# Optimization experiments

Hardware: AMD Instinct MI355X
Metric: run time of the kernel (lower is better)

The kernel has to match this reference:

```python
import jax, jax.numpy as jnp
import numpy as np

P_DROP = 0.2
N_NODES = 100000
N_EDGES = 1600000
IN_DIM, HID_DIM, OUT_DIM = 128, 128, 64


def sage_conv(x, src, dst, Wl, Wr, b, n_nodes):
    # PyG SAGEConv (aggr='mean', root_weight=True):
    #   out_i = W_l @ mean_{j in N(i)} x_j + W_r @ x_i + b
    msgs = jnp.take(x, src, axis=0)                                   # [E, d]
    agg = jax.ops.segment_sum(msgs, dst, num_segments=n_nodes)        # [N, d]
    cnt = jax.ops.segment_sum(jnp.ones((src.shape[0],), x.dtype), dst,
                              num_segments=n_nodes)                   # [N]
    agg = agg / jnp.maximum(cnt, 1.0)[:, None]                        # mean, 0 for isolated nodes
    return agg @ Wl + x @ Wr + b


def setup_inputs() -> dict:
    key = jax.random.key(0)
    ks = jax.random.split(key, 8)
    x = jax.random.normal(ks[0], (N_NODES, IN_DIM), dtype=jnp.float32)
    edge_index = jax.random.randint(ks[1], (2, N_EDGES), 0, N_NODES, dtype=jnp.int32)
    drop_u = jax.random.uniform(ks[2], (N_NODES, HID_DIM), dtype=jnp.float32)
    s1 = 1.0 / np.sqrt(IN_DIM)
    s2 = 1.0 / np.sqrt(HID_DIM)
    W1l = jax.random.normal(ks[3], (IN_DIM, HID_DIM), dtype=jnp.float32) * s1
    W1r = jax.random.normal(ks[4], (IN_DIM, HID_DIM), dtype=jnp.float32) * s1
    b1 = jnp.zeros((HID_DIM,), dtype=jnp.float32)
    W2l = jax.random.normal(ks[5], (HID_DIM, OUT_DIM), dtype=jnp.float32) * s2
    W2r = jax.random.normal(ks[6], (HID_DIM, OUT_DIM), dtype=jnp.float32) * s2
    b2 = jnp.zeros((OUT_DIM,), dtype=jnp.float32)
    return {"x": x, "edge_index": edge_index, "drop_u": drop_u,
            "W1l": W1l, "W1r": W1r, "b1": b1,
            "W2l": W2l, "W2r": W2r, "b2": b2}


def reference(x, edge_index, drop_u, W1l, W1r, b1, W2l, W2r, b2):
    n = x.shape[0]
    src, dst = edge_index[0], edge_index[1]
    h = jax.nn.elu(sage_conv(x, src, dst, W1l, W1r, b1, n))
    keep = (drop_u >= P_DROP).astype(h.dtype) / (1.0 - P_DROP)  # inverted dropout, p=0.2
    h = h * keep
    h = jax.nn.elu(sage_conv(h, src, dst, W2l, W2r, b2, n))
    return h
```

## Files before the change

kernel.cpp:

```cpp
#include <hip/hip_runtime.h>
#include <cstdint>
#include <cstddef>

#define TPB 256
#define BCAP 2560
#define NBKMAX 800
#define EPB 8192

typedef short bf16x8 __attribute__((ext_vector_type(8)));
typedef float f32x4 __attribute__((ext_vector_type(4)));

__device__ __forceinline__ unsigned short f2bf(float f) {
  unsigned int u = __float_as_uint(f);
  unsigned int r = (u + 0x7fffu + ((u >> 16) & 1u)) >> 16;
  return (unsigned short)r;
}
__device__ __forceinline__ float bf2f(unsigned short h) {
  return __uint_as_float(((unsigned int)h) << 16);
}

__device__ __forceinline__ void gload16(const void* g, void* l) {
  __builtin_amdgcn_global_load_lds(
      (const __attribute__((address_space(1))) unsigned int*)g,
      (__attribute__((address_space(3))) unsigned int*)l, 16, 0, 0);
}

template <int N>
__device__ __forceinline__ void waitvm() {
  asm volatile("s_waitcnt vmcnt(%0)" ::"n"(N) : "memory");
}


__global__ __launch_bounds__(256) void multisplit_scatter(
    const int* __restrict__ src, const int* __restrict__ dst,
    unsigned int* __restrict__ be, int* __restrict__ bcnt, int e, int nbk) {
  __shared__ int hist[NBKMAX];
  __shared__ int curs[NBKMAX];
  int tx = threadIdx.x;
  int e0 = blockIdx.x * EPB;
  int e1 = min(e, e0 + EPB);

  for (int b = tx; b < nbk; b += TPB) hist[b] = 0;
  __syncthreads();
  for (int i = e0 + tx; i < e1; i += TPB) atomicAdd(&hist[dst[i] >> 7], 1);
  __syncthreads();
  int rot = (blockIdx.x * 131) % nbk;
  for (int s = tx; s < nbk; s += TPB) {
    int b = s + rot;
    if (b >= nbk) b -= nbk;
    int h = hist[b];
    curs[b] = (h > 0) ? atomicAdd(&bcnt[b], h) : 0;
  }
  __syncthreads();
  for (int i = e0 + tx; i < e1; i += TPB) {
    int d = dst[i];
    int b = d >> 7;
    int p = atomicAdd(&curs[b], 1);
    if (p < BCAP)
      be[(size_t)b * BCAP + p] = ((unsigned int)(d & 127) << 17) | (unsigned int)src[i];
  }
}

__global__ void bucket_scan(const int* __restrict__ bcnt, int* __restrict__ bbase, int nbk) {
  __shared__ int s[TPB];
  __shared__ int carry;
  int tx = threadIdx.x;
  if (tx == 0) carry = 0;
  __syncthreads();
  for (int base = 0; base < nbk; base += TPB) {
    int i = base + tx;
    int v = (i < nbk) ? bcnt[i] : 0;
    s[tx] = v;
    __syncthreads();
    for (int d = 1; d < TPB; d <<= 1) {
      int t = (tx >= d) ? s[tx - d] : 0;
      __syncthreads();
      s[tx] += t;
      __syncthreads();
    }
    int c = carry;
    if (i < nbk) bbase[i] = c + s[tx] - v;
    __syncthreads();
    if (tx == TPB - 1) carry = c + s[tx];
    __syncthreads();
  }
}

__global__ __launch_bounds__(256) void per_bucket_build(
    const unsigned int* __restrict__ be, const int* __restrict__ bcnt,
    const int* __restrict__ bbase, int* __restrict__ off, int* __restrict__ col,
    int n, int e) {
  int b = blockIdx.x, tx = threadIdx.x;
  int cnt = bcnt[b];
  if (cnt > BCAP) cnt = BCAP;
  int base = bbase[b];
  int node0 = b << 7;
  __shared__ int scnt[128];
  __shared__ int sscan[128];
  if (tx < 128) scnt[tx] = 0;
  __syncthreads();
  const unsigned int* eb = be + (size_t)b * BCAP;
  for (int i = tx; i < cnt; i += 256) atomicAdd(&scnt[eb[i] >> 17], 1);
  __syncthreads();
  if (tx < 128) sscan[tx] = scnt[tx];
  __syncthreads();
  for (int d = 1; d < 128; d <<= 1) {
    int t = 0;
    if (tx < 128 && tx >= d) t = sscan[tx - d];
    __syncthreads();
    if (tx < 128) sscan[tx] += t;
    __syncthreads();
  }
  if (tx < 128) {
    int excl = sscan[tx] - scnt[tx];
    if (node0 + tx < n) off[node0 + tx] = base + excl;
    scnt[tx] = excl;
  }
  if (b == 0 && tx == 0) off[n] = e;
  __syncthreads();
  for (int i = tx; i < cnt; i += 256) {
    unsigned int u = eb[i];
    int p = atomicAdd(&scnt[u >> 17], 1);
    col[base + p] = (int)(u & 0x1ffff);
  }
}


__global__ void f32_to_bf16_v4(const float* __restrict__ in, unsigned short* __restrict__ out,
                               int n4) {
  int i = blockIdx.x * TPB + threadIdx.x;
  if (i >= n4) return;
  float4 v = ((const float4*)in)[i];
  ushort4 o;
  o.x = f2bf(v.x); o.y = f2bf(v.y); o.z = f2bf(v.z); o.w = f2bf(v.w);
  ((ushort4*)out)[i] = o;
}

__global__ void make_dropmask(const float* __restrict__ u, unsigned char* __restrict__ m,
                              int n4) {
  int i = blockIdx.x * TPB + threadIdx.x;
  if (i >= n4) return;
  float4 v = ((const float4*)u)[i];
  uchar4 o;
  o.x = (v.x >= 0.2f) ? 1 : 0;
  o.y = (v.y >= 0.2f) ? 1 : 0;
  o.z = (v.z >= 0.2f) ? 1 : 0;
  o.w = (v.w >= 0.2f) ? 1 : 0;
  ((uchar4*)m)[i] = o;
}

template <int NF>
__global__ void build_wt(const float* __restrict__ Wl, const float* __restrict__ Wr,
                         unsigned short* __restrict__ Wt) {
  int idx = blockIdx.x * TPB + threadIdx.x;
  if (idx >= NF * 256) return;
  int nn = idx >> 8;
  int k = idx & 255;
  float v = (k < 128) ? Wl[k * NF + nn] : Wr[(k - 128) * NF + nn];
  Wt[idx] = f2bf(v);
}


__global__ void aggregate_bf(const unsigned short* __restrict__ X,
                             const int* __restrict__ off, const int* __restrict__ col,
                             unsigned short* __restrict__ out, int n) {
  int node = (blockIdx.x * TPB + threadIdx.x) >> 6;
  int lane = threadIdx.x & 63;
  if (node >= n) return;
  int s0 = off[node], s1 = off[node + 1];
  float ax = 0.f, ay = 0.f;
  int e = s0;
  for (; e + 4 <= s1; e += 4) {
    int c0 = col[e], c1 = col[e + 1], c2 = col[e + 2], c3 = col[e + 3];
    unsigned int v0 = *(const unsigned int*)(X + (size_t)c0 * 128 + lane * 2);
    unsigned int v1 = *(const unsigned int*)(X + (size_t)c1 * 128 + lane * 2);
    unsigned int v2 = *(const unsigned int*)(X + (size_t)c2 * 128 + lane * 2);
    unsigned int v3 = *(const unsigned int*)(X + (size_t)c3 * 128 + lane * 2);
    ax += bf2f(v0 & 0xffff) + bf2f(v1 & 0xffff) + bf2f(v2 & 0xffff) + bf2f(v3 & 0xffff);
    ay += bf2f(v0 >> 16) + bf2f(v1 >> 16) + bf2f(v2 >> 16) + bf2f(v3 >> 16);
  }
  for (; e < s1; ++e) {
    int c = col[e];
    unsigned int v = *(const unsigned int*)(X + (size_t)c * 128 + lane * 2);
    ax += bf2f(v & 0xffff);
    ay += bf2f(v >> 16);
  }
  float inv = (s1 > s0) ? 1.0f / (float)(s1 - s0) : 0.f;
  unsigned int o = ((unsigned int)f2bf(ay * inv) << 16) | f2bf(ax * inv);
  *(unsigned int*)(out + (size_t)node * 128 + lane * 2) = o;
}


template <int NT, bool DROP, bool OUT32>
__global__ __launch_bounds__(256) void gemm_mfma(
    const unsigned short* __restrict__ A1, const unsigned short* __restrict__ A2,
    const unsigned short* __restrict__ Wt, const float* __restrict__ bias,
    const unsigned char* __restrict__ dmask, unsigned short* __restrict__ outb,
    float* __restrict__ outf, int n) {
  constexpr int NF = 32 * NT;
  constexpr int IPC = 4 + NT;
  __shared__ __align__(16) unsigned short sA[2][128 * 64];
  __shared__ __align__(16) unsigned short sB[2][NF * 64];

  int tid = threadIdx.x;
  int row0 = blockIdx.x * 128;
  int lane = tid & 63;
  int wid = tid >> 6;
  int wm = wid >> 1, wn = wid & 1;
  int lq = lane & 15, q = lane >> 4;

  int sr = tid >> 3, sc8 = tid & 7;
  int cg = sc8 ^ (sr & 7);

  int arow[4];
#pragma unroll
  for (int t = 0; t < 4; ++t) arow[t] = min(row0 + sr + t * 32, n - 1);

  f32x4 acc[4][NT];
#pragma unroll
  for (int i = 0; i < 4; ++i)
#pragma unroll
    for (int j = 0; j < NT; ++j) acc[i][j] = (f32x4)(0.f);

  auto issue = [&](int c, int b) {
    const unsigned short* Asrc = (c < 2) ? A1 : A2;
    int koff = (c & 1) * 64;
#pragma unroll
    for (int t = 0; t < 4; ++t) {
      gload16(Asrc + (size_t)arow[t] * 128 + koff + cg * 8,
              (char*)sA[b] + t * 4096 + wid * 1024);
    }
#pragma unroll
    for (int t = 0; t < NT; ++t) {
      gload16(Wt + (size_t)(sr + t * 32) * 256 + c * 64 + cg * 8,
              (char*)sB[b] + t * 4096 + wid * 1024);
    }
  };

  issue(0, 0);
  issue(1, 1);

#pragma unroll
  for (int c = 0; c < 4; ++c) {
    if (c < 3) waitvm<IPC>(); else waitvm<0>();
    __builtin_amdgcn_s_barrier();
    __builtin_amdgcn_sched_barrier(0);

    const int buf = c & 1;
#pragma unroll
    for (int ks = 0; ks < 2; ++ks) {
      bf16x8 a[4], b[NT];
#pragma unroll
      for (int i = 0; i < 4; ++i) {
        int rr = wm * 64 + i * 16 + lq;
        a[i] = *(const bf16x8*)(&sA[buf][rr * 64 + (((ks * 4 + q) ^ (rr & 7)) * 8)]);
      }
#pragma unroll
      for (int j = 0; j < NT; ++j) {
        int rb = wn * NT * 16 + j * 16 + lq;
        b[j] = *(const bf16x8*)(&sB[buf][rb * 64 + (((ks * 4 + q) ^ (rb & 7)) * 8)]);
      }
#pragma unroll
      for (int i = 0; i < 4; ++i)
#pragma unroll
        for (int j = 0; j < NT; ++j)
          acc[i][j] = __builtin_amdgcn_mfma_f32_16x16x32_bf16(a[i], b[j], acc[i][j], 0, 0, 0);
    }

    if (c < 2) {
      asm volatile("s_waitcnt lgkmcnt(0)" ::: "memory");
      __builtin_amdgcn_sched_barrier(0);
      __builtin_amdgcn_s_barrier();
      issue(c + 2, buf);
    }
  }

#pragma unroll
  for (int j = 0; j < NT; ++j) {
    int colg = wn * NT * 16 + j * 16 + lq;
    float bv = bias[colg];
#pragma unroll
    for (int i = 0; i < 4; ++i) {
      int rbase = row0 + wm * 64 + i * 16 + q * 4;
#pragma unroll
      for (int r = 0; r < 4; ++r) {
        int row = rbase + r;
        if (row >= n) continue;
        float v = acc[i][j][r] + bv;
        v = (v > 0.f) ? v : expm1f(v);
        if (DROP) {
          unsigned char k = dmask[(size_t)row * 128 + colg];
          v = k ? v * 1.25f : 0.f;
        }
        if (OUT32) outf[(size_t)row * NF + colg] = v;
        else outb[(size_t)row * NF + colg] = f2bf(v);
      }
    }
  }
}


extern "C" void kernel_launch(void* const* d_in, const int* in_sizes, int n_in,
                              void* d_out, int out_size, void* d_ws, size_t ws_size,
                              hipStream_t stream) {
  const float* x = (const float*)d_in[0];
  const int* ei = (const int*)d_in[1];
  const float* dropu = (const float*)d_in[2];
  const float* W1l = (const float*)d_in[3];
  const float* W1r = (const float*)d_in[4];
  const float* b1 = (const float*)d_in[5];
  const float* W2l = (const float*)d_in[6];
  const float* W2r = (const float*)d_in[7];
  const float* b2 = (const float*)d_in[8];

  int n = in_sizes[0] / 128;
  int e = in_sizes[1] / 2;
  const int* src = ei;
  const int* dst = ei + e;
  float* out = (float*)d_out;

  char* w = (char*)d_ws;
  auto alloc = [&](size_t bytes) -> char* {
    char* p = w;
    w += (bytes + 255) & ~(size_t)255;
    return p;
  };
  int nbk = (n + 127) / 128;
  int* off = (int*)alloc((size_t)(n + 1) * sizeof(int));
  int* col = (int*)alloc((size_t)e * sizeof(int));
  int* bcnt = (int*)alloc((size_t)nbk * sizeof(int));
  int* bbase = (int*)alloc((size_t)nbk * sizeof(int));
  unsigned short* xb = (unsigned short*)alloc((size_t)n * 128 * 2);
  unsigned short* hb = (unsigned short*)alloc((size_t)n * 128 * 2);
  unsigned short* aggb = (unsigned short*)alloc((size_t)n * 128 * 2);
  unsigned char* dmask = (unsigned char*)alloc((size_t)n * 128);
  unsigned short* Wt1 = (unsigned short*)alloc(128 * 256 * 2);
  unsigned short* Wt2 = (unsigned short*)alloc(64 * 256 * 2);
  unsigned int* be = (unsigned int*)aggb;

  hipMemsetAsync(bcnt, 0, (size_t)nbk * sizeof(int), stream);

  int gMS = (e + EPB - 1) / EPB;
  multisplit_scatter<<<gMS, TPB, 0, stream>>>(src, dst, be, bcnt, e, nbk);
  bucket_scan<<<1, TPB, 0, stream>>>(bcnt, bbase, nbk);
  per_bucket_build<<<nbk, TPB, 0, stream>>>(be, bcnt, bbase, off, col, n, e);

  int n4 = n * 128 / 4;
  f32_to_bf16_v4<<<(n4 + TPB - 1) / TPB, TPB, 0, stream>>>(x, xb, n4);
  make_dropmask<<<(n4 + TPB - 1) / TPB, TPB, 0, stream>>>(dropu, dmask, n4);
  build_wt<128><<<(128 * 256 + TPB - 1) / TPB, TPB, 0, stream>>>(W1l, W1r, Wt1);
  build_wt<64><<<(64 * 256 + TPB - 1) / TPB, TPB, 0, stream>>>(W2l, W2r, Wt2);

  int gN = (n + 3) / 4;
  int gR = (n + 127) / 128;

  aggregate_bf<<<gN, TPB, 0, stream>>>(xb, off, col, aggb, n);
  gemm_mfma<4, true, false><<<gR, TPB, 0, stream>>>(aggb, xb, Wt1, b1, dmask, hb, nullptr, n);

  aggregate_bf<<<gN, TPB, 0, stream>>>(hb, off, col, aggb, n);
  gemm_mfma<2, false, true><<<gR, TPB, 0, stream>>>(aggb, hb, Wt2, b2, nullptr, nullptr, out, n);
}
```

Before: 454.9 us.

## Aggregate four nodes per wavefront with 16-byte gathers and shuffled column indices

The mean-aggregation kernel now maps 16 lanes to each node, so a wavefront handles four nodes, and each lane loads 8 bf16 values with a single uint4 load. Neighbor indices are loaded cooperatively, 16 at a time, and broadcast with width-16 shuffles. A masked, fully unrolled 16-iteration loop then accumulates into 8 registers, and the grid is shrunk by a factor of four. This is meant to cut per-wave launch and index-load overhead and to raise memory-level parallelism. In exchange, the padding slots of partial 16-edge groups still issue redundant loads (masked to zero) for low-degree nodes.

```diff
diff --git a/kernel.cpp b/kernel.cpp
--- a/kernel.cpp
+++ b/kernel.cpp
@@ -164,30 +164,51 @@
 __global__ void aggregate_bf(const unsigned short* __restrict__ X,
                              const int* __restrict__ off, const int* __restrict__ col,
                              unsigned short* __restrict__ out, int n) {
-  int node = (blockIdx.x * TPB + threadIdx.x) >> 6;
+  int wv = (blockIdx.x * TPB + threadIdx.x) >> 6;
   int lane = threadIdx.x & 63;
-  if (node >= n) return;
-  int s0 = off[node], s1 = off[node + 1];
-  float ax = 0.f, ay = 0.f;
-  int e = s0;
-  for (; e + 4 <= s1; e += 4) {
-    int c0 = col[e], c1 = col[e + 1], c2 = col[e + 2], c3 = col[e + 3];
-    unsigned int v0 = *(const unsigned int*)(X + (size_t)c0 * 128 + lane * 2);
-    unsigned int v1 = *(const unsigned int*)(X + (size_t)c1 * 128 + lane * 2);
-    unsigned int v2 = *(const unsigned int*)(X + (size_t)c2 * 128 + lane * 2);
-    unsigned int v3 = *(const unsigned int*)(X + (size_t)c3 * 128 + lane * 2);
-    ax += bf2f(v0 & 0xffff) + bf2f(v1 & 0xffff) + bf2f(v2 & 0xffff) + bf2f(v3 & 0xffff);
-    ay += bf2f(v0 >> 16) + bf2f(v1 >> 16) + bf2f(v2 >> 16) + bf2f(v3 >> 16);
-  }
-  for (; e < s1; ++e) {
-    int c = col[e];
-    unsigned int v = *(const unsigned int*)(X + (size_t)c * 128 + lane * 2);
-    ax += bf2f(v & 0xffff);
-    ay += bf2f(v >> 16);
-  }
-  float inv = (s1 > s0) ? 1.0f / (float)(s1 - s0) : 0.f;
-  unsigned int o = ((unsigned int)f2bf(ay * inv) << 16) | f2bf(ax * inv);
-  *(unsigned int*)(out + (size_t)node * 128 + lane * 2) = o;
+  int li = lane & 15;
+  int node = wv * 4 + (lane >> 4);
+  bool alive = node < n;
+  int s0 = 0, s1 = 0;
+  if (alive) {
+    s0 = off[node];
+    s1 = off[node + 1];
+  }
+  int cnt = s1 - s0;
+
+  float a0 = 0.f, a1 = 0.f, a2 = 0.f, a3 = 0.f,
+        a4 = 0.f, a5 = 0.f, a6 = 0.f, a7 = 0.f;
+
+  for (int base = 0; base < cnt; base += 16) {
+    int idx = s0 + base + li;
+    int ci = col[min(idx, s1 - 1)];
+    int lim = cnt - base;
+#pragma unroll
+    for (int j = 0; j < 16; ++j) {
+      int c = __shfl(ci, j, 16);
+      const uint4* p = (const uint4*)(X + (size_t)c * 128 + li * 8);
+      uint4 v = *p;
+      float s = (j < lim) ? 1.f : 0.f;
+      a0 = fmaf(s, __uint_as_float(v.x << 16), a0);
+      a1 = fmaf(s, __uint_as_float(v.x & 0xffff0000u), a1);
+      a2 = fmaf(s, __uint_as_float(v.y << 16), a2);
+      a3 = fmaf(s, __uint_as_float(v.y & 0xffff0000u), a3);
+      a4 = fmaf(s, __uint_as_float(v.z << 16), a4);
+      a5 = fmaf(s, __uint_as_float(v.z & 0xffff0000u), a5);
+      a6 = fmaf(s, __uint_as_float(v.w << 16), a6);
+      a7 = fmaf(s, __uint_as_float(v.w & 0xffff0000u), a7);
+    }
+  }
+
+  if (alive) {
+    float inv = (cnt > 0) ? 1.0f / (float)cnt : 0.f;
+    uint4 o;
+    o.x = ((unsigned int)f2bf(a1 * inv) << 16) | f2bf(a0 * inv);
+    o.y = ((unsigned int)f2bf(a3 * inv) << 16) | f2bf(a2 * inv);
+    o.z = ((unsigned int)f2bf(a5 * inv) << 16) | f2bf(a4 * inv);
+    o.w = ((unsigned int)f2bf(a7 * inv) << 16) | f2bf(a6 * inv);
+    *(uint4*)(out + (size_t)node * 128 + li * 8) = o;
+  }
 }
 
 
@@ -351,12 +372,12 @@
   build_wt<128><<<(128 * 256 + TPB - 1) / TPB, TPB, 0, stream>>>(W1l, W1r, Wt1);
   build_wt<64><<<(64 * 256 + TPB - 1) / TPB, TPB, 0, stream>>>(W2l, W2r, Wt2);
 
-  int gN = (n + 3) / 4;
+  int gAgg = ((n + 3) / 4 * 64 + TPB - 1) / TPB;
   int gR = (n + 127) / 128;
 
-  aggregate_bf<<<gN, TPB, 0, stream>>>(xb, off, col, aggb, n);
+  aggregate_bf<<<gAgg, TPB, 0, stream>>>(xb, off, col, aggb, n);
   gemm_mfma<4, true, false><<<gR, TPB, 0, stream>>>(aggb, xb, Wt1, b1, dmask, hb, nullptr, n);
 
-  aggregate_bf<<<gN, TPB, 0, stream>>>(hb, off, col, aggb, n);
+  aggregate_bf<<<gAgg, TPB, 0, stream>>>(hb, off, col, aggb, n);
   gemm_mfma<2, false, true><<<gR, TPB, 0, stream>>>(aggb, hb, Wt2, b2, nullptr, nullptr, out, n);
 }
```

Measured after the change: 450.7 us. Within noise of the previous version (-0.9%).
